# Kernel tuning notes

Measured on AMD Instinct MI355X. Metric: run time of the kernel, lower is better.

The kernel has to match this reference:

```python
import jax, jax.numpy as jnp
import numpy as np

N, K, G = 4096, 4096, 128  # out_features, in_features, groupsize


def setup_inputs() -> dict:
    key = jax.random.key(0)
    k1, k2, k3, k4 = jax.random.split(key, 4)
    input = jax.random.normal(k1, (1, 2048, K), dtype=jnp.float32)
    # packed int4 weights: each byte holds two 4-bit codes (high nibble = even k, low = odd k)
    weight_packed = jax.random.randint(k2, (N, K // 2), 0, 256, dtype=jnp.int32)
    scales = jax.random.uniform(k3, (K // G, N), dtype=jnp.float32) * 0.02 + 1e-3
    zeros = jax.random.normal(k4, (K // G, N), dtype=jnp.float32) * 0.05
    scales_and_zeros = jnp.stack([scales, zeros], axis=-1)  # (K//G, N, 2)
    return {"input": input, "weight_packed": weight_packed,
            "scales_and_zeros": scales_and_zeros, "groupsize": G}


def reference(input, weight_packed, scales_and_zeros, groupsize):
    n, k_half = weight_packed.shape
    k = 2 * k_half
    g = k // groupsize
    # unpack two int4 codes per byte: high nibble first (even k index), then low nibble
    hi = (weight_packed >> 4) & 0xF
    lo = weight_packed & 0xF
    q = jnp.stack([hi, lo], axis=-1).reshape(n, k)  # (N, K), codes in [0,15]
    scales = scales_and_zeros[..., 0].T  # (N, G)
    zeros = scales_and_zeros[..., 1].T   # (N, G)
    # group-wise affine dequant: w = (q - 8) * scale + zero
    qg = q.reshape(n, g, groupsize).astype(jnp.float32)
    w = (qg - 8.0) * scales[:, :, None] + zeros[:, :, None]  # (N, G, gs)
    w = w.reshape(n, k)
    # out[..., n] = sum_k input[..., k] * w[n, k]
    return jnp.einsum('bsk,nk->bsn', input, w)
```

## Files before the change

kernel.cpp:

```cpp
#include <hip/hip_runtime.h>
#include <hip/hip_bf16.h>


using bf16x8 = __attribute__((ext_vector_type(8))) short;
using f32x16 = __attribute__((ext_vector_type(16))) float;

#define KK 4096
#define NN 4096
#define NT (KK / 64)

static __device__ __forceinline__ short f2bf(float f) {
    __hip_bfloat16 h = __float2bfloat16(f);
    return __builtin_bit_cast(short, h);
}

#define GLDS16(gptr, lptr) __builtin_amdgcn_global_load_lds( \
    (const __attribute__((address_space(1))) void*)(gptr),   \
    (__attribute__((address_space(3))) void*)(lptr), 16, 0, 0)

#define MFMA32 __builtin_amdgcn_mfma_f32_32x32x16_bf16
#define SBAR() __builtin_amdgcn_sched_barrier(0)

static __device__ __forceinline__ bf16x8 dq8(int4 p, float s, float zs) {
    bf16x8 r;
    int v[4] = {p.x, p.y, p.z, p.w};
    #pragma unroll
    for (int j = 0; j < 4; ++j) {
        r[2 * j]     = f2bf((float)((v[j] >> 4) & 0xF) * s + zs);
        r[2 * j + 1] = f2bf((float)(v[j] & 0xF) * s + zs);
    }
    return r;
}

__global__ __launch_bounds__(256) void cvt_a(
    const float* __restrict__ A, short* __restrict__ Ab)
{
    const int idx = blockIdx.x * 256 + threadIdx.x;
    const float4* s = (const float4*)(A + (size_t)idx * 8);
    float4 u = s[0], v = s[1];
    bf16x8 r;
    r[0] = f2bf(u.x); r[1] = f2bf(u.y); r[2] = f2bf(u.z); r[3] = f2bf(u.w);
    r[4] = f2bf(v.x); r[5] = f2bf(v.y); r[6] = f2bf(v.z); r[7] = f2bf(v.w);
    *(bf16x8*)&Ab[(size_t)idx * 8] = r;
}

__global__ __launch_bounds__(512, 2) void gemm_fq(
    const short* __restrict__ Ab, const int* __restrict__ W,
    const float* __restrict__ SZ, float* __restrict__ C)
{
    __shared__ short sA[3 * 256 * 64];
    __shared__ short sB[3 * 128 * 64];

    const int tid  = threadIdx.x;
    const int lane = tid & 63;
    const int wave = tid >> 6;
    const int wm   = wave >> 1;
    const int wn   = wave & 1;
    const int bm   = blockIdx.y * 256;
    const int bn   = blockIdx.x * 128;

    const int sl = lane >> 3;
    const int sc = (lane & 7) ^ sl;
    const short* aSt = Ab + (size_t)(bm + wave * 32 + sl) * KK + sc * 8;

    const int brow = wave * 16 + (lane >> 2);
    const int bl4  = lane & 3;
    const int* wSt = W + (size_t)(bn + brow) * (KK / 2) + bl4 * 8;
    const float* szp = SZ + (size_t)(bn + brow) * 2;
    const int bw0 = brow * 64 + (((bl4 * 2))     ^ (brow & 7)) * 8;
    const int bw1 = brow * 64 + (((bl4 * 2) | 1) ^ (brow & 7)) * 8;

    const int l31 = lane & 31;
    const int lx  = lane >> 5;
    const int l7  = lane & 7;
    const int px0 = ((0 + lx) ^ l7) * 8;
    const int px1 = ((2 + lx) ^ l7) * 8;
    const int px2 = ((4 + lx) ^ l7) * 8;
    const int px3 = ((6 + lx) ^ l7) * 8;
    const int aRd = (wm * 64 + l31) * 64;
    const int bRd = (wn * 64 + l31) * 64;

    f32x16 acc00 = {}, acc01 = {}, acc10 = {}, acc11 = {};
    bf16x8 pA00, pA01, pA10, pA11, pB00, pB01, pB10, pB11;
    bf16x8 qA00, qA01, qA10, qA11, qB00, qB01, qB10, qB11;

    int4 b00p = *(const int4*)(wSt + 0);
    int4 b01p = *(const int4*)(wSt + 4);
    float2 sz0 = *(const float2*)(szp);
    int4 b10p = *(const int4*)(wSt + 32);
    int4 b11p = *(const int4*)(wSt + 36);
    #pragma unroll
    for (int l = 0; l < 4; ++l)
        GLDS16(aSt + (size_t)l * 8 * KK,      &sA[(wave * 32 + l * 8) * 64]);
    #pragma unroll
    for (int l = 0; l < 4; ++l)
        GLDS16(aSt + (size_t)l * 8 * KK + 64, &sA[16384 + (wave * 32 + l * 8) * 64]);
    {
        const float s = sz0.x, zs = sz0.y - 8.0f * sz0.x;
        *(bf16x8*)&sB[bw0]        = dq8(b00p, s, zs);
        *(bf16x8*)&sB[bw1]        = dq8(b01p, s, zs);
        *(bf16x8*)&sB[8192 + bw0] = dq8(b10p, s, zs);
        *(bf16x8*)&sB[8192 + bw1] = dq8(b11p, s, zs);
    }
    asm volatile("s_waitcnt vmcnt(4)" ::: "memory");
    asm volatile("s_waitcnt lgkmcnt(0)" ::: "memory");
    __builtin_amdgcn_s_barrier();

    pA00 = *(const bf16x8*)&sA[aRd + px0];
    pA01 = *(const bf16x8*)&sA[aRd + px1];
    pA10 = *(const bf16x8*)&sA[aRd + 2048 + px0];
    pA11 = *(const bf16x8*)&sA[aRd + 2048 + px1];
    pB00 = *(const bf16x8*)&sB[bRd + px0];
    pB01 = *(const bf16x8*)&sB[bRd + px1];
    pB10 = *(const bf16x8*)&sB[bRd + 2048 + px0];
    pB11 = *(const bf16x8*)&sB[bRd + 2048 + px1];
    asm volatile("s_waitcnt lgkmcnt(0)" ::: "memory");
    SBAR();

    int cur = 0;
    for (int t = 0; t < NT; ++t) {
        const int nxt1 = (cur == 2) ? 0 : cur + 1;
        const int nxt2 = (nxt1 == 2) ? 0 : nxt1 + 1;
        const short* sAc = &sA[cur * 16384];
        const short* sBc = &sB[cur * 8192];
        const short* sA1 = &sA[nxt1 * 16384];
        const short* sB1 = &sB[nxt1 * 8192];
        short* sAn = &sA[nxt2 * 16384];
        short* sBn = &sB[nxt2 * 8192];
        const bool st = (t + 2 < NT);
        const int gk = (t + 2) * 64;

        qA00 = *(const bf16x8*)&sAc[aRd + px2];
        qA01 = *(const bf16x8*)&sAc[aRd + px3];
        qA10 = *(const bf16x8*)&sAc[aRd + 2048 + px2];
        qA11 = *(const bf16x8*)&sAc[aRd + 2048 + px3];
        qB00 = *(const bf16x8*)&sBc[bRd + px2];
        qB01 = *(const bf16x8*)&sBc[bRd + px3];
        qB10 = *(const bf16x8*)&sBc[bRd + 2048 + px2];
        qB11 = *(const bf16x8*)&sBc[bRd + 2048 + px3];
        int4 bp0, bp1; float2 szv;
        if (st) {
            bp0 = *(const int4*)(wSt + (gk >> 1));
            bp1 = *(const int4*)(wSt + (gk >> 1) + 4);
            szv = *(const float2*)(szp + (size_t)((t + 2) >> 1) * NN * 2);
            GLDS16(aSt + (size_t)0 * 8 * KK + gk, sAn + (wave * 32 + 0) * 64);
            GLDS16(aSt + (size_t)1 * 8 * KK + gk, sAn + (wave * 32 + 8) * 64);
            GLDS16(aSt + (size_t)2 * 8 * KK + gk, sAn + (wave * 32 + 16) * 64);
            GLDS16(aSt + (size_t)3 * 8 * KK + gk, sAn + (wave * 32 + 24) * 64);
        }
        SBAR();

        __builtin_amdgcn_s_setprio(1);
        acc00 = MFMA32(pA00, pB00, acc00, 0, 0, 0);
        acc00 = MFMA32(pA01, pB01, acc00, 0, 0, 0);
        acc01 = MFMA32(pA00, pB10, acc01, 0, 0, 0);
        acc01 = MFMA32(pA01, pB11, acc01, 0, 0, 0);
        acc10 = MFMA32(pA10, pB00, acc10, 0, 0, 0);
        acc10 = MFMA32(pA11, pB01, acc10, 0, 0, 0);
        acc11 = MFMA32(pA10, pB10, acc11, 0, 0, 0);
        acc11 = MFMA32(pA11, pB11, acc11, 0, 0, 0);
        __builtin_amdgcn_s_setprio(0);

        if (st) {
            asm volatile("s_waitcnt vmcnt(4)" ::: "memory");
        } else {
            asm volatile("s_waitcnt vmcnt(0)" ::: "memory");
        }
        SBAR();
        if (st) {
            const float s = szv.x, zs = szv.y - 8.0f * szv.x;
            *(bf16x8*)&sBn[bw0] = dq8(bp0, s, zs);
            *(bf16x8*)&sBn[bw1] = dq8(bp1, s, zs);
        }
        asm volatile("s_waitcnt lgkmcnt(0)" ::: "memory");
        SBAR();
        __builtin_amdgcn_s_barrier();

        if (t + 1 < NT) {
            pA00 = *(const bf16x8*)&sA1[aRd + px0];
            pA01 = *(const bf16x8*)&sA1[aRd + px1];
            pA10 = *(const bf16x8*)&sA1[aRd + 2048 + px0];
            pA11 = *(const bf16x8*)&sA1[aRd + 2048 + px1];
            pB00 = *(const bf16x8*)&sB1[bRd + px0];
            pB01 = *(const bf16x8*)&sB1[bRd + px1];
            pB10 = *(const bf16x8*)&sB1[bRd + 2048 + px0];
            pB11 = *(const bf16x8*)&sB1[bRd + 2048 + px1];
        }
        SBAR();

        __builtin_amdgcn_s_setprio(1);
        acc00 = MFMA32(qA00, qB00, acc00, 0, 0, 0);
        acc00 = MFMA32(qA01, qB01, acc00, 0, 0, 0);
        acc01 = MFMA32(qA00, qB10, acc01, 0, 0, 0);
        acc01 = MFMA32(qA01, qB11, acc01, 0, 0, 0);
        acc10 = MFMA32(qA10, qB00, acc10, 0, 0, 0);
        acc10 = MFMA32(qA11, qB01, acc10, 0, 0, 0);
        acc11 = MFMA32(qA10, qB10, acc11, 0, 0, 0);
        acc11 = MFMA32(qA11, qB11, acc11, 0, 0, 0);
        __builtin_amdgcn_s_setprio(0);

        asm volatile("s_waitcnt lgkmcnt(0)" ::: "memory");
        SBAR();

        cur = nxt1;
    }

    {
        const int crow = lx * 4;
        float* Cp = C + (size_t)(bm + wm * 64) * NN + bn + wn * 64;
        #pragma unroll
        for (int m = 0; m < 2; ++m) {
            #pragma unroll
            for (int qr = 0; qr < 4; ++qr) {
                #pragma unroll
                for (int j = 0; j < 4; ++j) {
                    const int row = m * 32 + crow + j + 8 * qr;
                    float* dst = Cp + (size_t)row * NN + l31;
                    if (m == 0) {
                        dst[0]  = acc00[qr * 4 + j];
                        dst[32] = acc01[qr * 4 + j];
                    } else {
                        dst[0]  = acc10[qr * 4 + j];
                        dst[32] = acc11[qr * 4 + j];
                    }
                }
            }
        }
    }
}

using f32x4 = __attribute__((ext_vector_type(4))) float;
#define LDKF 72
__global__ __launch_bounds__(256) void wq4_gemm_fused(
    const float* __restrict__ A, const int* __restrict__ W,
    const float* __restrict__ SZ, float* __restrict__ C, int M)
{
    __shared__ short sA[128 * LDKF];
    __shared__ short sB[128 * LDKF];
    const int tid = threadIdx.x, lane = tid & 63, wave = tid >> 6;
    const int wr = (wave >> 1) << 6, wc = (wave & 1) << 6;
    const int bm = blockIdx.y * 128, bn = blockIdx.x * 128;
    const int ar = tid >> 2, ac = (tid & 3) << 4;
    const int br = tid >> 1, bh = (tid & 1) << 4;
    const float* Arow0 = A + (size_t)(bm + ar) * KK + ac;
    const float* Arow1 = A + (size_t)(bm + 64 + ar) * KK + ac;
    const int*   Wrow  = W + (size_t)(bn + br) * (KK / 2) + bh;
    const float* SZrow = SZ + (size_t)(bn + br) * 2;
    f32x4 acc[4][4] = {};
    for (int k0 = 0; k0 < KK; k0 += 64) {
        {
            const float4* s0 = (const float4*)(Arow0 + k0);
            const float4* s1 = (const float4*)(Arow1 + k0);
            float4 a0 = s0[0], a1 = s0[1], a2 = s0[2], a3 = s0[3];
            float4 b0 = s1[0], b1 = s1[1], b2 = s1[2], b3 = s1[3];
            auto cvt8 = [](float4 u, float4 v) -> bf16x8 {
                bf16x8 r;
                r[0] = f2bf(u.x); r[1] = f2bf(u.y); r[2] = f2bf(u.z); r[3] = f2bf(u.w);
                r[4] = f2bf(v.x); r[5] = f2bf(v.y); r[6] = f2bf(v.z); r[7] = f2bf(v.w);
                return r;
            };
            *(bf16x8*)&sA[ar * LDKF + ac]            = cvt8(a0, a1);
            *(bf16x8*)&sA[ar * LDKF + ac + 8]        = cvt8(a2, a3);
            *(bf16x8*)&sA[(64 + ar) * LDKF + ac]     = cvt8(b0, b1);
            *(bf16x8*)&sA[(64 + ar) * LDKF + ac + 8] = cvt8(b2, b3);
        }
        {
            const int g = k0 >> 7;
            const float2 sz = *(const float2*)(SZrow + (size_t)g * NN * 2);
            const float scale = sz.x, zs = sz.y - 8.0f * sz.x;
            const int4* src = (const int4*)(Wrow + (k0 >> 1));
            #pragma unroll
            for (int i = 0; i < 4; ++i) {
                int4 p = src[i];
                int vals[4] = {p.x, p.y, p.z, p.w};
                bf16x8 r;
                #pragma unroll
                for (int j = 0; j < 4; ++j) {
                    int v = vals[j];
                    r[2 * j]     = f2bf((float)((v >> 4) & 0xF) * scale + zs);
                    r[2 * j + 1] = f2bf((float)(v & 0xF) * scale + zs);
                }
                *(bf16x8*)&sB[br * LDKF + (bh << 1) + (i << 3)] = r;
            }
        }
        __syncthreads();
        #pragma unroll
        for (int ks = 0; ks < 2; ++ks) {
            const int col = (ks << 5) + ((lane >> 4) << 3);
            bf16x8 af[4], bfr[4];
            #pragma unroll
            for (int m = 0; m < 4; ++m)
                af[m] = *(const bf16x8*)&sA[(wr + m * 16 + (lane & 15)) * LDKF + col];
            #pragma unroll
            for (int n = 0; n < 4; ++n)
                bfr[n] = *(const bf16x8*)&sB[(wc + n * 16 + (lane & 15)) * LDKF + col];
            #pragma unroll
            for (int m = 0; m < 4; ++m)
                #pragma unroll
                for (int n = 0; n < 4; ++n)
                    acc[m][n] = __builtin_amdgcn_mfma_f32_16x16x32_bf16(
                        af[m], bfr[n], acc[m][n], 0, 0, 0);
        }
        __syncthreads();
    }
    float* Cp = C + (size_t)(bm + wr) * NN + bn + wc;
    const int cr = (lane >> 4) << 2, cc = lane & 15;
    #pragma unroll
    for (int m = 0; m < 4; ++m)
        #pragma unroll
        for (int j = 0; j < 4; ++j) {
            float* dst = Cp + (size_t)(m * 16 + cr + j) * NN + cc;
            #pragma unroll
            for (int n = 0; n < 4; ++n) dst[n * 16] = acc[m][n][j];
        }
}

extern "C" void kernel_launch(void* const* d_in, const int* in_sizes, int n_in,
                              void* d_out, int out_size, void* d_ws, size_t ws_size,
                              hipStream_t stream) {
    const float* A  = (const float*)d_in[0];
    const int*   W  = (const int*)d_in[1];
    const float* SZ = (const float*)d_in[2];
    float* C = (float*)d_out;

    const int M = in_sizes[0] / KK;

    const size_t ab_elems = (size_t)M * KK;
    const size_t need = ab_elems * sizeof(short);

    if (ws_size >= need && (M % 256) == 0) {
        short* Ab = (short*)d_ws;
        cvt_a<<<(int)(ab_elems / 8 / 256), 256, 0, stream>>>(A, Ab);
        dim3 grid(NN / 128, M / 256);
        gemm_fq<<<grid, dim3(512), 0, stream>>>(Ab, W, SZ, C);
    } else {
        dim3 grid(NN / 128, M / 128);
        wq4_gemm_fused<<<grid, dim3(256), 0, stream>>>(A, W, SZ, C, M);
    }
}
```

Baseline: 104.0 us.

## Prefetch packed int4 weights one extra tile ahead with ping-pong registers

Packed weight and scale/zero loads are now issued one tile earlier (t+3) into alternating register sets, unrolling the K loop by two so each half uses a fixed register set. The dequantize-and-store to LDS happens after the barrier, overlapping it with the second MFMA half, and the global weight-load latency gets a full iteration to hide. This adds register pressure from the extra int4/float2 prefetch registers and reorders the vmcnt waits, which could affect occupancy at the two-blocks-per-CU launch bound.

```diff
diff --git a/kernel.cpp b/kernel.cpp
--- a/kernel.cpp
+++ b/kernel.cpp
@@ -44,7 +44,7 @@
     *(bf16x8*)&Ab[(size_t)idx * 8] = r;
 }
 
-__global__ __launch_bounds__(512, 2) void gemm_fq(
+__global__ __launch_bounds__(512, 2) void gemm_fq2(
     const short* __restrict__ Ab, const int* __restrict__ W,
     const float* __restrict__ SZ, float* __restrict__ C)
 {
@@ -83,26 +83,30 @@
     f32x16 acc00 = {}, acc01 = {}, acc10 = {}, acc11 = {};
     bf16x8 pA00, pA01, pA10, pA11, pB00, pB01, pB10, pB11;
     bf16x8 qA00, qA01, qA10, qA11, qB00, qB01, qB10, qB11;
-
-    int4 b00p = *(const int4*)(wSt + 0);
-    int4 b01p = *(const int4*)(wSt + 4);
-    float2 sz0 = *(const float2*)(szp);
-    int4 b10p = *(const int4*)(wSt + 32);
-    int4 b11p = *(const int4*)(wSt + 36);
+    int4 bpE0, bpE1, bpO0, bpO1; float2 szE, szO;
+
+    int4 w0a = *(const int4*)(wSt + 0);
+    int4 w0b = *(const int4*)(wSt + 4);
+    int4 w1a = *(const int4*)(wSt + 32);
+    int4 w1b = *(const int4*)(wSt + 36);
+    float2 sz01 = *(const float2*)(szp);
     #pragma unroll
     for (int l = 0; l < 4; ++l)
         GLDS16(aSt + (size_t)l * 8 * KK,      &sA[(wave * 32 + l * 8) * 64]);
     #pragma unroll
     for (int l = 0; l < 4; ++l)
         GLDS16(aSt + (size_t)l * 8 * KK + 64, &sA[16384 + (wave * 32 + l * 8) * 64]);
+    bpE0 = *(const int4*)(wSt + 64);
+    bpE1 = *(const int4*)(wSt + 68);
+    szE  = *(const float2*)(szp + (size_t)NN * 2);
     {
-        const float s = sz0.x, zs = sz0.y - 8.0f * sz0.x;
-        *(bf16x8*)&sB[bw0]        = dq8(b00p, s, zs);
-        *(bf16x8*)&sB[bw1]        = dq8(b01p, s, zs);
-        *(bf16x8*)&sB[8192 + bw0] = dq8(b10p, s, zs);
-        *(bf16x8*)&sB[8192 + bw1] = dq8(b11p, s, zs);
-    }
-    asm volatile("s_waitcnt vmcnt(4)" ::: "memory");
+        const float s = sz01.x, zs = sz01.y - 8.0f * sz01.x;
+        *(bf16x8*)&sB[bw0]        = dq8(w0a, s, zs);
+        *(bf16x8*)&sB[bw1]        = dq8(w0b, s, zs);
+        *(bf16x8*)&sB[8192 + bw0] = dq8(w1a, s, zs);
+        *(bf16x8*)&sB[8192 + bw1] = dq8(w1b, s, zs);
+    }
+    asm volatile("s_waitcnt vmcnt(7)" ::: "memory");
     asm volatile("s_waitcnt lgkmcnt(0)" ::: "memory");
     __builtin_amdgcn_s_barrier();
 
@@ -118,92 +122,96 @@
     SBAR();
 
     int cur = 0;
-    for (int t = 0; t < NT; ++t) {
-        const int nxt1 = (cur == 2) ? 0 : cur + 1;
-        const int nxt2 = (nxt1 == 2) ? 0 : nxt1 + 1;
-        const short* sAc = &sA[cur * 16384];
-        const short* sBc = &sB[cur * 8192];
-        const short* sA1 = &sA[nxt1 * 16384];
-        const short* sB1 = &sB[nxt1 * 8192];
-        short* sAn = &sA[nxt2 * 16384];
-        short* sBn = &sB[nxt2 * 8192];
-        const bool st = (t + 2 < NT);
-        const int gk = (t + 2) * 64;
-
-        qA00 = *(const bf16x8*)&sAc[aRd + px2];
-        qA01 = *(const bf16x8*)&sAc[aRd + px3];
-        qA10 = *(const bf16x8*)&sAc[aRd + 2048 + px2];
-        qA11 = *(const bf16x8*)&sAc[aRd + 2048 + px3];
-        qB00 = *(const bf16x8*)&sBc[bRd + px2];
-        qB01 = *(const bf16x8*)&sBc[bRd + px3];
-        qB10 = *(const bf16x8*)&sBc[bRd + 2048 + px2];
-        qB11 = *(const bf16x8*)&sBc[bRd + 2048 + px3];
-        int4 bp0, bp1; float2 szv;
-        if (st) {
-            bp0 = *(const int4*)(wSt + (gk >> 1));
-            bp1 = *(const int4*)(wSt + (gk >> 1) + 4);
-            szv = *(const float2*)(szp + (size_t)((t + 2) >> 1) * NN * 2);
-            GLDS16(aSt + (size_t)0 * 8 * KK + gk, sAn + (wave * 32 + 0) * 64);
-            GLDS16(aSt + (size_t)1 * 8 * KK + gk, sAn + (wave * 32 + 8) * 64);
-            GLDS16(aSt + (size_t)2 * 8 * KK + gk, sAn + (wave * 32 + 16) * 64);
-            GLDS16(aSt + (size_t)3 * 8 * KK + gk, sAn + (wave * 32 + 24) * 64);
-        }
-        SBAR();
-
-        __builtin_amdgcn_s_setprio(1);
-        acc00 = MFMA32(pA00, pB00, acc00, 0, 0, 0);
-        acc00 = MFMA32(pA01, pB01, acc00, 0, 0, 0);
-        acc01 = MFMA32(pA00, pB10, acc01, 0, 0, 0);
-        acc01 = MFMA32(pA01, pB11, acc01, 0, 0, 0);
-        acc10 = MFMA32(pA10, pB00, acc10, 0, 0, 0);
-        acc10 = MFMA32(pA11, pB01, acc10, 0, 0, 0);
-        acc11 = MFMA32(pA10, pB10, acc11, 0, 0, 0);
-        acc11 = MFMA32(pA11, pB11, acc11, 0, 0, 0);
-        __builtin_amdgcn_s_setprio(0);
-
-        if (st) {
-            asm volatile("s_waitcnt vmcnt(4)" ::: "memory");
-        } else {
-            asm volatile("s_waitcnt vmcnt(0)" ::: "memory");
-        }
-        SBAR();
-        if (st) {
-            const float s = szv.x, zs = szv.y - 8.0f * szv.x;
-            *(bf16x8*)&sBn[bw0] = dq8(bp0, s, zs);
-            *(bf16x8*)&sBn[bw1] = dq8(bp1, s, zs);
-        }
-        asm volatile("s_waitcnt lgkmcnt(0)" ::: "memory");
-        SBAR();
-        __builtin_amdgcn_s_barrier();
-
-        if (t + 1 < NT) {
-            pA00 = *(const bf16x8*)&sA1[aRd + px0];
-            pA01 = *(const bf16x8*)&sA1[aRd + px1];
-            pA10 = *(const bf16x8*)&sA1[aRd + 2048 + px0];
-            pA11 = *(const bf16x8*)&sA1[aRd + 2048 + px1];
-            pB00 = *(const bf16x8*)&sB1[bRd + px0];
-            pB01 = *(const bf16x8*)&sB1[bRd + px1];
-            pB10 = *(const bf16x8*)&sB1[bRd + 2048 + px0];
-            pB11 = *(const bf16x8*)&sB1[bRd + 2048 + px1];
-        }
-        SBAR();
-
-        __builtin_amdgcn_s_setprio(1);
-        acc00 = MFMA32(qA00, qB00, acc00, 0, 0, 0);
-        acc00 = MFMA32(qA01, qB01, acc00, 0, 0, 0);
-        acc01 = MFMA32(qA00, qB10, acc01, 0, 0, 0);
-        acc01 = MFMA32(qA01, qB11, acc01, 0, 0, 0);
-        acc10 = MFMA32(qA10, qB00, acc10, 0, 0, 0);
-        acc10 = MFMA32(qA11, qB01, acc10, 0, 0, 0);
-        acc11 = MFMA32(qA10, qB10, acc11, 0, 0, 0);
-        acc11 = MFMA32(qA11, qB11, acc11, 0, 0, 0);
-        __builtin_amdgcn_s_setprio(0);
-
-        asm volatile("s_waitcnt lgkmcnt(0)" ::: "memory");
-        SBAR();
-
-        cur = nxt1;
-    }
+
+#define TILE_BODY(T, BPW0, BPW1, SZW, BPL0, BPL1, SZL)                        \
+    {                                                                         \
+        const int nxt1 = (cur == 2) ? 0 : cur + 1;                            \
+        const int nxt2 = (nxt1 == 2) ? 0 : nxt1 + 1;                          \
+        const short* sAc = &sA[cur * 16384];                                  \
+        const short* sBc = &sB[cur * 8192];                                   \
+        const short* sA1 = &sA[nxt1 * 16384];                                 \
+        const short* sB1 = &sB[nxt1 * 8192];                                  \
+        short* sAn = &sA[nxt2 * 16384];                                       \
+        short* sBn = &sB[nxt2 * 8192];                                        \
+        const bool st = ((T) + 2 < NT);                                       \
+        const int gk = ((T) + 2) * 64;                                        \
+                                   \
+        qA00 = *(const bf16x8*)&sAc[aRd + px2];                               \
+        qA01 = *(const bf16x8*)&sAc[aRd + px3];                               \
+        qA10 = *(const bf16x8*)&sAc[aRd + 2048 + px2];                        \
+        qA11 = *(const bf16x8*)&sAc[aRd + 2048 + px3];                        \
+        qB00 = *(const bf16x8*)&sBc[bRd + px2];                               \
+        qB01 = *(const bf16x8*)&sBc[bRd + px3];                               \
+        qB10 = *(const bf16x8*)&sBc[bRd + 2048 + px2];                        \
+        qB11 = *(const bf16x8*)&sBc[bRd + 2048 + px3];                        \
+        if (st) {                                                             \
+            GLDS16(aSt + (size_t)0 * 8 * KK + gk, sAn + (wave * 32 + 0) * 64);\
+            GLDS16(aSt + (size_t)1 * 8 * KK + gk, sAn + (wave * 32 + 8) * 64);\
+            GLDS16(aSt + (size_t)2 * 8 * KK + gk, sAn + (wave * 32 + 16) * 64);\
+            GLDS16(aSt + (size_t)3 * 8 * KK + gk, sAn + (wave * 32 + 24) * 64);\
+        }                                                                     \
+        SBAR();                                                               \
+        __builtin_amdgcn_s_setprio(1);                                        \
+        acc00 = MFMA32(pA00, pB00, acc00, 0, 0, 0);                           \
+        acc00 = MFMA32(pA01, pB01, acc00, 0, 0, 0);                           \
+        acc01 = MFMA32(pA00, pB10, acc01, 0, 0, 0);                           \
+        acc01 = MFMA32(pA01, pB11, acc01, 0, 0, 0);                           \
+        acc10 = MFMA32(pA10, pB00, acc10, 0, 0, 0);                           \
+        acc10 = MFMA32(pA11, pB01, acc10, 0, 0, 0);                           \
+        acc11 = MFMA32(pA10, pB10, acc11, 0, 0, 0);                           \
+        acc11 = MFMA32(pA11, pB11, acc11, 0, 0, 0);                           \
+        __builtin_amdgcn_s_setprio(0);                                        \
+                            \
+        asm volatile("s_waitcnt lgkmcnt(0)" ::: "memory");                    \
+        SBAR();                                                               \
+        if (st) {                                                             \
+            asm volatile("s_waitcnt vmcnt(4)" ::: "memory");                  \
+        } else {                                                              \
+            asm volatile("s_waitcnt vmcnt(0)" ::: "memory");                  \
+        }                                                                     \
+        __builtin_amdgcn_s_barrier();                                         \
+                    \
+        if ((T) + 1 < NT) {                                                   \
+            pA00 = *(const bf16x8*)&sA1[aRd + px0];                           \
+            pA01 = *(const bf16x8*)&sA1[aRd + px1];                           \
+            pA10 = *(const bf16x8*)&sA1[aRd + 2048 + px0];                    \
+            pA11 = *(const bf16x8*)&sA1[aRd + 2048 + px1];                    \
+            pB00 = *(const bf16x8*)&sB1[bRd + px0];                           \
+            pB01 = *(const bf16x8*)&sB1[bRd + px1];                           \
+            pB10 = *(const bf16x8*)&sB1[bRd + 2048 + px0];                    \
+            pB11 = *(const bf16x8*)&sB1[bRd + 2048 + px1];                    \
+        }                                                                     \
+        if ((T) + 3 < NT) {                                                   \
+            BPL0 = *(const int4*)(wSt + (((T) + 3) * 32));                    \
+            BPL1 = *(const int4*)(wSt + (((T) + 3) * 32) + 4);                \
+            SZL  = *(const float2*)(szp + (size_t)(((T) + 3) >> 1) * NN * 2); \
+        }                                                                     \
+        if (st) {                                                             \
+            const float s = SZW.x, zs = SZW.y - 8.0f * SZW.x;                 \
+            *(bf16x8*)&sBn[bw0] = dq8(BPW0, s, zs);                           \
+            *(bf16x8*)&sBn[bw1] = dq8(BPW1, s, zs);                           \
+        }                                                                     \
+        SBAR();                                                               \
+        __builtin_amdgcn_s_setprio(1);                                        \
+        acc00 = MFMA32(qA00, qB00, acc00, 0, 0, 0);                           \
+        acc00 = MFMA32(qA01, qB01, acc00, 0, 0, 0);                           \
+        acc01 = MFMA32(qA00, qB10, acc01, 0, 0, 0);                           \
+        acc01 = MFMA32(qA01, qB11, acc01, 0, 0, 0);                           \
+        acc10 = MFMA32(qA10, qB00, acc10, 0, 0, 0);                           \
+        acc10 = MFMA32(qA11, qB01, acc10, 0, 0, 0);                           \
+        acc11 = MFMA32(qA10, qB10, acc11, 0, 0, 0);                           \
+        acc11 = MFMA32(qA11, qB11, acc11, 0, 0, 0);                           \
+        __builtin_amdgcn_s_setprio(0);                                        \
+        asm volatile("s_waitcnt lgkmcnt(0)" ::: "memory");                    \
+        SBAR();                                                               \
+        cur = nxt1;                                                           \
+    }
+
+    for (int t = 0; t < NT; t += 2) {
+        TILE_BODY(t,     bpE0, bpE1, szE, bpO0, bpO1, szO);
+        TILE_BODY(t + 1, bpO0, bpO1, szO, bpE0, bpE1, szE);
+    }
+#undef TILE_BODY
 
     {
         const int crow = lx * 4;
@@ -332,7 +340,7 @@
         short* Ab = (short*)d_ws;
         cvt_a<<<(int)(ab_elems / 8 / 256), 256, 0, stream>>>(A, Ab);
         dim3 grid(NN / 128, M / 256);
-        gemm_fq<<<grid, dim3(512), 0, stream>>>(Ab, W, SZ, C);
+        gemm_fq2<<<grid, dim3(512), 0, stream>>>(Ab, W, SZ, C);
     } else {
         dim3 grid(NN / 128, M / 128);
         wq4_gemm_fused<<<grid, dim3(256), 0, stream>>>(A, W, SZ, C, M);
```

After: 99.19 us. -4.6%, faster.
